# Performance work log

Hardware: AMD Instinct MI355X
Metric: run time of the kernel (lower is better)

Reference implementation:

```python
import jax, jax.numpy as jnp
import numpy as np

B, T, U, OUT_STEPS = 64, 128, 1024, 16


def setup_inputs() -> dict:
    key = jax.random.key(0)
    ks = jax.random.split(key, 8)
    s = 0.05  # small init scale to keep gates out of saturation
    return {
        "inputs": jax.random.normal(ks[0], (B, T, 1), jnp.float32),
        "k1": jax.random.normal(ks[1], (1, 4 * U), jnp.float32) * s,
        "r1": jax.random.normal(ks[2], (U, 4 * U), jnp.float32) * s,
        "b1": jnp.zeros((4 * U,), jnp.float32),
        "k2": jax.random.normal(ks[3], (U, 4 * U), jnp.float32) * s,
        "r2": jax.random.normal(ks[4], (U, 4 * U), jnp.float32) * s,
        "b2": jnp.zeros((4 * U,), jnp.float32),
        "wd": jax.random.normal(ks[5], (U, 1), jnp.float32) * s,
        "bd": jnp.zeros((1,), jnp.float32),
        "out_steps": OUT_STEPS,
    }


def _lstm(x_seq, h0, c0, Wx, Wh, b):
    """Keras-ordered (i,f,g,o) LSTM over a [B,T,D] sequence via lax.scan."""
    def step(carry, xt):
        h, c = carry
        z = xt @ Wx + h @ Wh + b  # [B, 4U]
        i, f, g, o = jnp.split(z, 4, axis=-1)
        c = jax.nn.sigmoid(f) * c + jax.nn.sigmoid(i) * jnp.tanh(g)
        h = jax.nn.sigmoid(o) * jnp.tanh(c)
        return (h, c), h
    (h, c), ys = jax.lax.scan(step, (h0, c0), jnp.swapaxes(x_seq, 0, 1))
    return jnp.swapaxes(ys, 0, 1), h, c  # seq [B,T,U], final h, c


def reference(inputs, k1, r1, b1, k2, r2, b2, wd, bd, out_steps):
    Bn = inputs.shape[0]
    Un = r1.shape[0]
    z0 = jnp.zeros((Bn, Un), inputs.dtype)
    # warmup: only lstm2's final states survive (faithful to the source code)
    x, _, _ = _lstm(inputs, z0, z0, k1, r1, b1)
    x, h, c = _lstm(x, z0, z0, k2, r2, b2)
    pred = x @ wd + bd  # [B, T, 1] (Dense applied to full sequence)
    preds = [pred]
    for _ in range(1, out_steps):
        # source quirk: lstm1 is seeded with lstm2's previous states,
        # lstm2 is seeded with lstm1's current states
        x, h1, c1 = _lstm(pred, h, c, k1, r1, b1)
        x, h, c = _lstm(x, h1, c1, k2, r2, b2)
        pred = x @ wd + bd
        preds.append(pred)
    return jnp.concatenate(preds, axis=1)  # [B, out_steps*T, 1]
```

## Files before the change

kernel.cpp:

```cpp
#include <hip/hip_runtime.h>
#include <cstdint>
#include <cstddef>

#define UU 1024
#define FOURU 4096
#define BATCH 64
#define TTT 128
#define SSS 16

typedef __attribute__((ext_vector_type(8))) short short8;
typedef __attribute__((ext_vector_type(4))) float f32x4;

__device__ __forceinline__ unsigned short f2bf(float f) {
    union { float f; uint32_t u; } v; v.f = f;
    uint32_t u = v.u;
    uint32_t r = (u + 0x7fffu + ((u >> 16) & 1u)) >> 16;
    return (unsigned short)r;
}
__device__ __forceinline__ float bf2f(unsigned short h) {
    union { uint32_t u; float f; } v; v.u = ((uint32_t)h) << 16;
    return v.f;
}

__global__ void repack_w1(const float* __restrict__ r1,
                          unsigned short* __restrict__ whi,
                          unsigned short* __restrict__ wlo) {
    int idx = blockIdx.x * 256 + threadIdx.x;
    int pc = idx >> 10, k = idx & 1023;
    int b = pc >> 4, g = (pc >> 2) & 3, j = pc & 3;
    int oc = g * UU + b * 4 + j;
    float v = r1[(size_t)k * FOURU + oc];
    unsigned short hi = f2bf(v);
    whi[idx] = hi;
    wlo[idx] = f2bf(v - bf2f(hi));
}

__global__ void repack_w2(const float* __restrict__ k2, const float* __restrict__ r2,
                          unsigned short* __restrict__ whi,
                          unsigned short* __restrict__ wlo) {
    int idx = blockIdx.x * 256 + threadIdx.x;
    int pc = idx >> 11, k = idx & 2047;
    int b = pc >> 4, g = (pc >> 2) & 3, j = pc & 3;
    int oc = g * UU + b * 4 + j;
    float v = (k < UU) ? k2[(size_t)k * FOURU + oc]
                       : r2[(size_t)(k - UU) * FOURU + oc];
    unsigned short hi = f2bf(v);
    whi[idx] = hi;
    wlo[idx] = f2bf(v - bf2f(hi));
}

template <int KTOT, bool IS1>
__global__ __launch_bounds__(256, 1) void cell_step(
    const unsigned short* __restrict__ Whi, const unsigned short* __restrict__ Wlo,
    const unsigned short* __restrict__ A1hi, const unsigned short* __restrict__ A1lo,
    const unsigned short* __restrict__ A2hi, const unsigned short* __restrict__ A2lo,
    const float* __restrict__ cin, float* __restrict__ cout,
    unsigned short* __restrict__ Hhi, unsigned short* __restrict__ Hlo,
    const float* __restrict__ bias,
    const float* __restrict__ k1, const float* __restrict__ xsrc, int xstride,
    int flags) {
    __shared__ float zp[4][64][16];
    const int tid = threadIdx.x;
    const int lane = tid & 63;
    const int w = tid >> 6;
    const int blk = blockIdx.x;
    constexpr int KSL = KTOT / 4;

    f32x4 acc[4] = {};

    bool skip;
    if (IS1) skip = (flags & 1) != 0;
    else     skip = ((flags & 1) != 0) && (w >= 2);

    if (!skip) {
        const int kbase = w * KSL;
        const unsigned short* Ah;
        const unsigned short* Al;
        int koff;
        if (KTOT == 2048 && kbase >= UU) { Ah = A2hi; Al = A2lo; koff = kbase - UU; }
        else                             { Ah = A1hi; Al = A1lo; koff = kbase; }
        const int kg8 = (lane >> 4) * 8;
        const int colpc = blk * 16 + (lane & 15);
        const unsigned short* wrh = Whi + (size_t)colpc * KTOT + kbase + kg8;
        const unsigned short* wrl = Wlo + (size_t)colpc * KTOT + kbase + kg8;

        for (int kk = 0; kk < KSL; kk += 32) {
            short8 bh = *(const short8*)(wrh + kk);
            short8 bl = *(const short8*)(wrl + kk);
#pragma unroll
            for (int m = 0; m < 4; ++m) {
                const int row = m * 16 + (lane & 15);
                const size_t aoff = (size_t)row * UU + koff + kk + kg8;
                short8 ah = *(const short8*)(Ah + aoff);
                short8 al = *(const short8*)(Al + aoff);
                acc[m] = __builtin_amdgcn_mfma_f32_16x16x32_bf16(ah, bh, acc[m], 0, 0, 0);
                acc[m] = __builtin_amdgcn_mfma_f32_16x16x32_bf16(al, bh, acc[m], 0, 0, 0);
                acc[m] = __builtin_amdgcn_mfma_f32_16x16x32_bf16(ah, bl, acc[m], 0, 0, 0);
            }
        }
    }

#pragma unroll
    for (int m = 0; m < 4; ++m) {
        const int rbase = m * 16 + (lane >> 4) * 4;
#pragma unroll
        for (int r = 0; r < 4; ++r)
            zp[w][rbase + r][lane & 15] = acc[m][r];
    }
    __syncthreads();

    {
        const int row = tid & 63;
        const int j = tid >> 6;
        float z[4];
#pragma unroll
        for (int g = 0; g < 4; ++g) {
            float s = 0.f;
#pragma unroll
            for (int ww = 0; ww < 4; ++ww) s += zp[ww][row][g * 4 + j];
            const int oc = g * UU + blk * 4 + j;
            s += bias[oc];
            if (IS1) {
                float xv = xsrc[(size_t)row * xstride];
                s += xv * k1[oc];
            }
            z[g] = s;
        }
        const int u = blk * 4 + j;
        float cold = (flags & 2) ? 0.f : cin[(size_t)row * UU + u];
        float ig = 1.f / (1.f + expf(-z[0]));
        float fg = 1.f / (1.f + expf(-z[1]));
        float gg = tanhf(z[2]);
        float og = 1.f / (1.f + expf(-z[3]));
        float cn = fg * cold + ig * gg;
        float hn = og * tanhf(cn);
        cout[(size_t)row * UU + u] = cn;
        unsigned short hh = f2bf(hn);
        Hhi[(size_t)row * UU + u] = hh;
        Hlo[(size_t)row * UU + u] = f2bf(hn - bf2f(hh));
    }
}

__global__ void dense_pred(const unsigned short* __restrict__ X2hi,
                           const unsigned short* __restrict__ X2lo,
                           const float* __restrict__ wd, const float* __restrict__ bd,
                           float* __restrict__ out) {
    const int gw = (blockIdx.x * 256 + threadIdx.x) >> 6;
    const int lane = threadIdx.x & 63;
    for (int d = gw; d < TTT * BATCH; d += 2048) {
        const int t = d >> 6, b = d & 63;
        const unsigned short* ph = X2hi + ((size_t)t * BATCH + b) * UU;
        const unsigned short* pl = X2lo + ((size_t)t * BATCH + b) * UU;
        float s = 0.f;
#pragma unroll 4
        for (int i = lane; i < UU; i += 64)
            s += (bf2f(ph[i]) + bf2f(pl[i])) * wd[i];
#pragma unroll
        for (int off = 32; off; off >>= 1) s += __shfl_down(s, off, 64);
        if (lane == 0) out[(size_t)b * (SSS * TTT) + t] = s + bd[0];
    }
}

extern "C" void kernel_launch(void* const* d_in, const int* in_sizes, int n_in,
                              void* d_out, int out_size, void* d_ws, size_t ws_size,
                              hipStream_t stream) {
    const float* inputs = (const float*)d_in[0];
    const float* k1     = (const float*)d_in[1];
    const float* r1     = (const float*)d_in[2];
    const float* b1     = (const float*)d_in[3];
    const float* k2     = (const float*)d_in[4];
    const float* r2     = (const float*)d_in[5];
    const float* b2     = (const float*)d_in[6];
    const float* wd     = (const float*)d_in[7];
    const float* bd     = (const float*)d_in[8];
    float* out = (float*)d_out;

    char* ws = (char*)d_ws;
    size_t off = 0;
    auto carve = [&](size_t bytes) -> void* {
        void* p = ws + off;
        off += (bytes + 255) & ~(size_t)255;
        return p;
    };
    const size_t BU = (size_t)BATCH * UU;
    unsigned short* W1hi = (unsigned short*)carve((size_t)FOURU * UU * 2);
    unsigned short* W1lo = (unsigned short*)carve((size_t)FOURU * UU * 2);
    unsigned short* W2hi = (unsigned short*)carve((size_t)FOURU * 2048 * 2);
    unsigned short* W2lo = (unsigned short*)carve((size_t)FOURU * 2048 * 2);
    unsigned short* X1hi = (unsigned short*)carve((size_t)TTT * BU * 2);
    unsigned short* X1lo = (unsigned short*)carve((size_t)TTT * BU * 2);
    unsigned short* X2hi = (unsigned short*)carve((size_t)TTT * BU * 2);
    unsigned short* X2lo = (unsigned short*)carve((size_t)TTT * BU * 2);
    float* c1 = (float*)carve(BU * 4);
    float* c2 = (float*)carve(BU * 4);

    repack_w1<<<dim3((FOURU * UU) / 256), dim3(256), 0, stream>>>(r1, W1hi, W1lo);
    repack_w2<<<dim3((FOURU * 2048) / 256), dim3(256), 0, stream>>>(k2, r2, W2hi, W2lo);

    for (int s = 0; s < SSS; ++s) {
        for (int t = 0; t < TTT; ++t) {
            const unsigned short *Ahi, *Alo;
            if (t == 0) { Ahi = X2hi + 127 * BU; Alo = X2lo + 127 * BU; }
            else        { Ahi = X1hi + (size_t)(t - 1) * BU; Alo = X1lo + (size_t)(t - 1) * BU; }
            const float* cinp = (t == 0) ? c2 : c1;
            int flags = (s == 0 && t == 0) ? 3 : 0;
            const float* xsrc;
            int xstride;
            if (s == 0) { xsrc = inputs + t; xstride = TTT; }
            else        { xsrc = out + (size_t)(s - 1) * TTT + t; xstride = SSS * TTT; }
            cell_step<1024, true><<<dim3(256), dim3(256), 0, stream>>>(
                W1hi, W1lo, Ahi, Alo, (const unsigned short*)nullptr, (const unsigned short*)nullptr,
                cinp, c1, X1hi + (size_t)t * BU, X1lo + (size_t)t * BU,
                b1, k1, xsrc, xstride, flags);
        }
        for (int t = 0; t < TTT; ++t) {
            const unsigned short *A2hi_, *A2lo_;
            if (t == 0) { A2hi_ = X1hi + 127 * BU; A2lo_ = X1lo + 127 * BU; }
            else        { A2hi_ = X2hi + (size_t)(t - 1) * BU; A2lo_ = X2lo + (size_t)(t - 1) * BU; }
            const float* cinp = (t == 0) ? c1 : c2;
            int flags = (s == 0 && t == 0) ? 3 : 0;
            cell_step<2048, false><<<dim3(256), dim3(256), 0, stream>>>(
                W2hi, W2lo,
                X1hi + (size_t)t * BU, X1lo + (size_t)t * BU, A2hi_, A2lo_,
                cinp, c2, X2hi + (size_t)t * BU, X2lo + (size_t)t * BU,
                b2, (const float*)nullptr, (const float*)nullptr, 0, flags);
        }
        dense_pred<<<dim3(512), dim3(256), 0, stream>>>(X2hi, X2lo, wd, bd,
                                                        out + (size_t)s * TTT);
    }
}
```

Before: 79.94 ms.

## Replace per-timestep launches with one persistent kernel using grid barriers

Replaces the ~4100 per-timestep kernel launches with a single persistent kernel of 256 blocks that loops over all steps, synchronising through an atomic grid barrier. The split-bf16 weight slices are kept in registers for the whole run instead of being reloaded from memory each step, and cell states move from global memory into registers. The dense prediction is folded into the same kernel. In exchange it needs all 256 blocks co-resident and holds 96 short8 vectors of weights per thread, which risks register spills, and the spin-based barrier adds latency on every step.

```diff
diff --git a/kernel.cpp b/kernel.cpp
--- a/kernel.cpp
+++ b/kernel.cpp
@@ -7,6 +7,8 @@
 #define BATCH 64
 #define TTT 128
 #define SSS 16
+#define BU 65536
+#define NBLK 256
 
 typedef __attribute__((ext_vector_type(8))) short short8;
 typedef __attribute__((ext_vector_type(4))) float f32x4;
@@ -20,6 +22,27 @@
 __device__ __forceinline__ float bf2f(unsigned short h) {
     union { uint32_t u; float f; } v; v.u = ((uint32_t)h) << 16;
     return v.f;
+}
+
+__device__ __forceinline__ void grid_barrier(unsigned int* bar) {
+    __syncthreads();
+    if (threadIdx.x == 0) {
+        unsigned int g = __hip_atomic_load(bar + 16, __ATOMIC_RELAXED, __HIP_MEMORY_SCOPE_AGENT);
+        unsigned int a = __hip_atomic_fetch_add(bar, 1u, __ATOMIC_ACQ_REL, __HIP_MEMORY_SCOPE_AGENT);
+        if (a == NBLK - 1u) {
+            __hip_atomic_store(bar, 0u, __ATOMIC_RELAXED, __HIP_MEMORY_SCOPE_AGENT);
+            __hip_atomic_store(bar + 16, g + 1u, __ATOMIC_RELEASE, __HIP_MEMORY_SCOPE_AGENT);
+        } else {
+            while (__hip_atomic_load(bar + 16, __ATOMIC_ACQUIRE, __HIP_MEMORY_SCOPE_AGENT) == g) {
+                __builtin_amdgcn_s_sleep(1);
+            }
+        }
+    }
+    __syncthreads();
+}
+
+__global__ void bar_init(unsigned int* bar) {
+    bar[threadIdx.x] = 0u;
 }
 
 __global__ void repack_w1(const float* __restrict__ r1,
@@ -49,115 +72,188 @@
     wlo[idx] = f2bf(v - bf2f(hi));
 }
 
-template <int KTOT, bool IS1>
-__global__ __launch_bounds__(256, 1) void cell_step(
-    const unsigned short* __restrict__ Whi, const unsigned short* __restrict__ Wlo,
-    const unsigned short* __restrict__ A1hi, const unsigned short* __restrict__ A1lo,
-    const unsigned short* __restrict__ A2hi, const unsigned short* __restrict__ A2lo,
-    const float* __restrict__ cin, float* __restrict__ cout,
-    unsigned short* __restrict__ Hhi, unsigned short* __restrict__ Hlo,
-    const float* __restrict__ bias,
-    const float* __restrict__ k1, const float* __restrict__ xsrc, int xstride,
-    int flags) {
+__global__ __launch_bounds__(256, 1) void feedback_persistent(
+    const unsigned short* __restrict__ W1hi, const unsigned short* __restrict__ W1lo,
+    const unsigned short* __restrict__ W2hi, const unsigned short* __restrict__ W2lo,
+    unsigned short* __restrict__ X1hi, unsigned short* __restrict__ X1lo,
+    unsigned short* __restrict__ X2hi, unsigned short* __restrict__ X2lo,
+    const float* __restrict__ inputs, const float* __restrict__ k1,
+    const float* __restrict__ b1, const float* __restrict__ b2,
+    const float* __restrict__ wd, const float* __restrict__ bd,
+    float* __restrict__ out, unsigned int* bar) {
     __shared__ float zp[4][64][16];
+
     const int tid = threadIdx.x;
     const int lane = tid & 63;
     const int w = tid >> 6;
     const int blk = blockIdx.x;
-    constexpr int KSL = KTOT / 4;
-
-    f32x4 acc[4] = {};
-
-    bool skip;
-    if (IS1) skip = (flags & 1) != 0;
-    else     skip = ((flags & 1) != 0) && (w >= 2);
-
-    if (!skip) {
-        const int kbase = w * KSL;
-        const unsigned short* Ah;
-        const unsigned short* Al;
-        int koff;
-        if (KTOT == 2048 && kbase >= UU) { Ah = A2hi; Al = A2lo; koff = kbase - UU; }
-        else                             { Ah = A1hi; Al = A1lo; koff = kbase; }
-        const int kg8 = (lane >> 4) * 8;
-        const int colpc = blk * 16 + (lane & 15);
-        const unsigned short* wrh = Whi + (size_t)colpc * KTOT + kbase + kg8;
-        const unsigned short* wrl = Wlo + (size_t)colpc * KTOT + kbase + kg8;
-
-        for (int kk = 0; kk < KSL; kk += 32) {
-            short8 bh = *(const short8*)(wrh + kk);
-            short8 bl = *(const short8*)(wrl + kk);
+    const int kg8 = (lane >> 4) * 8;
+    const int colpc = blk * 16 + (lane & 15);
+
+    short8 w1h[8], w1l[8], w2h[16], w2l[16];
+    {
+        const size_t base1 = (size_t)colpc * 1024 + (size_t)w * 256 + kg8;
+#pragma unroll
+        for (int i = 0; i < 8; ++i) {
+            w1h[i] = *(const short8*)(W1hi + base1 + i * 32);
+            w1l[i] = *(const short8*)(W1lo + base1 + i * 32);
+        }
+        const size_t base2 = (size_t)colpc * 2048 + (size_t)w * 512 + kg8;
+#pragma unroll
+        for (int i = 0; i < 16; ++i) {
+            w2h[i] = *(const short8*)(W2hi + base2 + i * 32);
+            w2l[i] = *(const short8*)(W2lo + base2 + i * 32);
+        }
+    }
+
+    const int erow = tid >> 2;
+    const int ej = tid & 3;
+    const int eu = blk * 4 + ej;
+    float b1v[4], b2v[4], k1v[4];
+#pragma unroll
+    for (int g = 0; g < 4; ++g) {
+        const int oc = g * UU + blk * 4 + ej;
+        b1v[g] = b1[oc];
+        b2v[g] = b2[oc];
+        k1v[g] = k1[oc];
+    }
+    float c1 = 0.f, c2 = 0.f;
+
+    const int gw = blk * 4 + w;
+
+    for (int s = 0; s < SSS; ++s) {
+        for (int t = 0; t < TTT; ++t) {
+            f32x4 acc[4] = {};
+            if (!(s == 0 && t == 0)) {
+                const unsigned short *Ah, *Al;
+                if (t == 0) { Ah = X2hi + 127 * BU; Al = X2lo + 127 * BU; }
+                else        { Ah = X1hi + (size_t)(t - 1) * BU; Al = X1lo + (size_t)(t - 1) * BU; }
+                const int koff = w * 256;
+#pragma unroll
+                for (int i = 0; i < 8; ++i) {
+                    const int kk = i * 32;
+#pragma unroll
+                    for (int m = 0; m < 4; ++m) {
+                        const int row = m * 16 + (lane & 15);
+                        const size_t aoff = (size_t)row * UU + koff + kk + kg8;
+                        short8 ah = *(const short8*)(Ah + aoff);
+                        short8 al = *(const short8*)(Al + aoff);
+                        acc[m] = __builtin_amdgcn_mfma_f32_16x16x32_bf16(ah, w1h[i], acc[m], 0, 0, 0);
+                        acc[m] = __builtin_amdgcn_mfma_f32_16x16x32_bf16(al, w1h[i], acc[m], 0, 0, 0);
+                        acc[m] = __builtin_amdgcn_mfma_f32_16x16x32_bf16(ah, w1l[i], acc[m], 0, 0, 0);
+                    }
+                }
+            }
 #pragma unroll
             for (int m = 0; m < 4; ++m) {
-                const int row = m * 16 + (lane & 15);
-                const size_t aoff = (size_t)row * UU + koff + kk + kg8;
-                short8 ah = *(const short8*)(Ah + aoff);
-                short8 al = *(const short8*)(Al + aoff);
-                acc[m] = __builtin_amdgcn_mfma_f32_16x16x32_bf16(ah, bh, acc[m], 0, 0, 0);
-                acc[m] = __builtin_amdgcn_mfma_f32_16x16x32_bf16(al, bh, acc[m], 0, 0, 0);
-                acc[m] = __builtin_amdgcn_mfma_f32_16x16x32_bf16(ah, bl, acc[m], 0, 0, 0);
-            }
-        }
-    }
-
-#pragma unroll
-    for (int m = 0; m < 4; ++m) {
-        const int rbase = m * 16 + (lane >> 4) * 4;
-#pragma unroll
-        for (int r = 0; r < 4; ++r)
-            zp[w][rbase + r][lane & 15] = acc[m][r];
-    }
-    __syncthreads();
-
-    {
-        const int row = tid & 63;
-        const int j = tid >> 6;
-        float z[4];
-#pragma unroll
-        for (int g = 0; g < 4; ++g) {
-            float s = 0.f;
-#pragma unroll
-            for (int ww = 0; ww < 4; ++ww) s += zp[ww][row][g * 4 + j];
-            const int oc = g * UU + blk * 4 + j;
-            s += bias[oc];
-            if (IS1) {
-                float xv = xsrc[(size_t)row * xstride];
-                s += xv * k1[oc];
-            }
-            z[g] = s;
-        }
-        const int u = blk * 4 + j;
-        float cold = (flags & 2) ? 0.f : cin[(size_t)row * UU + u];
-        float ig = 1.f / (1.f + expf(-z[0]));
-        float fg = 1.f / (1.f + expf(-z[1]));
-        float gg = tanhf(z[2]);
-        float og = 1.f / (1.f + expf(-z[3]));
-        float cn = fg * cold + ig * gg;
-        float hn = og * tanhf(cn);
-        cout[(size_t)row * UU + u] = cn;
-        unsigned short hh = f2bf(hn);
-        Hhi[(size_t)row * UU + u] = hh;
-        Hlo[(size_t)row * UU + u] = f2bf(hn - bf2f(hh));
-    }
-}
-
-__global__ void dense_pred(const unsigned short* __restrict__ X2hi,
-                           const unsigned short* __restrict__ X2lo,
-                           const float* __restrict__ wd, const float* __restrict__ bd,
-                           float* __restrict__ out) {
-    const int gw = (blockIdx.x * 256 + threadIdx.x) >> 6;
-    const int lane = threadIdx.x & 63;
-    for (int d = gw; d < TTT * BATCH; d += 2048) {
-        const int t = d >> 6, b = d & 63;
-        const unsigned short* ph = X2hi + ((size_t)t * BATCH + b) * UU;
-        const unsigned short* pl = X2lo + ((size_t)t * BATCH + b) * UU;
-        float s = 0.f;
+                const int rbase = m * 16 + (lane >> 4) * 4;
+#pragma unroll
+                for (int r = 0; r < 4; ++r)
+                    zp[w][rbase + r][lane & 15] = acc[m][r];
+            }
+            __syncthreads();
+            {
+                float xv = (s == 0) ? inputs[(size_t)erow * TTT + t]
+                                    : out[(size_t)erow * (SSS * TTT) + (s - 1) * TTT + t];
+                float z[4];
+#pragma unroll
+                for (int g = 0; g < 4; ++g) {
+                    float sum = zp[0][erow][g * 4 + ej] + zp[1][erow][g * 4 + ej] +
+                                zp[2][erow][g * 4 + ej] + zp[3][erow][g * 4 + ej];
+                    z[g] = sum + b1v[g] + xv * k1v[g];
+                }
+                float cold = (t == 0) ? c2 : c1;
+                float ig = 1.f / (1.f + expf(-z[0]));
+                float fg = 1.f / (1.f + expf(-z[1]));
+                float gg = tanhf(z[2]);
+                float og = 1.f / (1.f + expf(-z[3]));
+                float cn = fg * cold + ig * gg;
+                float hn = og * tanhf(cn);
+                c1 = cn;
+                unsigned short hh = f2bf(hn);
+                const size_t hoff = (size_t)t * BU + (size_t)erow * UU + eu;
+                X1hi[hoff] = hh;
+                X1lo[hoff] = f2bf(hn - bf2f(hh));
+            }
+            grid_barrier(bar);
+        }
+        for (int t = 0; t < TTT; ++t) {
+            f32x4 acc[4] = {};
+            const bool skiph = (s == 0 && t == 0);
+            {
+                const unsigned short *Ah, *Al;
+                int koff;
+                if (w < 2) {
+                    Ah = X1hi + (size_t)t * BU;
+                    Al = X1lo + (size_t)t * BU;
+                    koff = w * 512;
+                } else {
+                    if (t == 0) { Ah = X1hi + 127 * BU; Al = X1lo + 127 * BU; }
+                    else        { Ah = X2hi + (size_t)(t - 1) * BU; Al = X2lo + (size_t)(t - 1) * BU; }
+                    koff = (w - 2) * 512;
+                }
+                if (!(skiph && w >= 2)) {
+#pragma unroll
+                    for (int i = 0; i < 16; ++i) {
+                        const int kk = i * 32;
+#pragma unroll
+                        for (int m = 0; m < 4; ++m) {
+                            const int row = m * 16 + (lane & 15);
+                            const size_t aoff = (size_t)row * UU + koff + kk + kg8;
+                            short8 ah = *(const short8*)(Ah + aoff);
+                            short8 al = *(const short8*)(Al + aoff);
+                            acc[m] = __builtin_amdgcn_mfma_f32_16x16x32_bf16(ah, w2h[i], acc[m], 0, 0, 0);
+                            acc[m] = __builtin_amdgcn_mfma_f32_16x16x32_bf16(al, w2h[i], acc[m], 0, 0, 0);
+                            acc[m] = __builtin_amdgcn_mfma_f32_16x16x32_bf16(ah, w2l[i], acc[m], 0, 0, 0);
+                        }
+                    }
+                }
+            }
+#pragma unroll
+            for (int m = 0; m < 4; ++m) {
+                const int rbase = m * 16 + (lane >> 4) * 4;
+#pragma unroll
+                for (int r = 0; r < 4; ++r)
+                    zp[w][rbase + r][lane & 15] = acc[m][r];
+            }
+            __syncthreads();
+            {
+                float z[4];
+#pragma unroll
+                for (int g = 0; g < 4; ++g) {
+                    float sum = zp[0][erow][g * 4 + ej] + zp[1][erow][g * 4 + ej] +
+                                zp[2][erow][g * 4 + ej] + zp[3][erow][g * 4 + ej];
+                    z[g] = sum + b2v[g];
+                }
+                float cold = (t == 0) ? ((s == 0) ? 0.f : c1) : c2;
+                float ig = 1.f / (1.f + expf(-z[0]));
+                float fg = 1.f / (1.f + expf(-z[1]));
+                float gg = tanhf(z[2]);
+                float og = 1.f / (1.f + expf(-z[3]));
+                float cn = fg * cold + ig * gg;
+                float hn = og * tanhf(cn);
+                c2 = cn;
+                unsigned short hh = f2bf(hn);
+                const size_t hoff = (size_t)t * BU + (size_t)erow * UU + eu;
+                X2hi[hoff] = hh;
+                X2lo[hoff] = f2bf(hn - bf2f(hh));
+            }
+            grid_barrier(bar);
+        }
+        for (int i = 0; i < 8; ++i) {
+            const int d = gw + 1024 * i;
+            const int t = d >> 6, b = d & 63;
+            const unsigned short* ph = X2hi + (size_t)t * BU + (size_t)b * UU;
+            const unsigned short* pl = X2lo + (size_t)t * BU + (size_t)b * UU;
+            float ssum = 0.f;
 #pragma unroll 4
-        for (int i = lane; i < UU; i += 64)
-            s += (bf2f(ph[i]) + bf2f(pl[i])) * wd[i];
-#pragma unroll
-        for (int off = 32; off; off >>= 1) s += __shfl_down(s, off, 64);
-        if (lane == 0) out[(size_t)b * (SSS * TTT) + t] = s + bd[0];
+            for (int ii = lane; ii < UU; ii += 64)
+                ssum += (bf2f(ph[ii]) + bf2f(pl[ii])) * wd[ii];
+#pragma unroll
+            for (int off = 32; off; off >>= 1) ssum += __shfl_down(ssum, off, 64);
+            if (lane == 0) out[(size_t)b * (SSS * TTT) + s * TTT + t] = ssum + bd[0];
+        }
+        grid_barrier(bar);
     }
 }
 
@@ -182,7 +278,6 @@
         off += (bytes + 255) & ~(size_t)255;
         return p;
     };
-    const size_t BU = (size_t)BATCH * UU;
     unsigned short* W1hi = (unsigned short*)carve((size_t)FOURU * UU * 2);
     unsigned short* W1lo = (unsigned short*)carve((size_t)FOURU * UU * 2);
     unsigned short* W2hi = (unsigned short*)carve((size_t)FOURU * 2048 * 2);
@@ -191,41 +286,13 @@
     unsigned short* X1lo = (unsigned short*)carve((size_t)TTT * BU * 2);
     unsigned short* X2hi = (unsigned short*)carve((size_t)TTT * BU * 2);
     unsigned short* X2lo = (unsigned short*)carve((size_t)TTT * BU * 2);
-    float* c1 = (float*)carve(BU * 4);
-    float* c2 = (float*)carve(BU * 4);
-
+    unsigned int* bar = (unsigned int*)carve(256);
+
+    bar_init<<<dim3(1), dim3(64), 0, stream>>>(bar);
     repack_w1<<<dim3((FOURU * UU) / 256), dim3(256), 0, stream>>>(r1, W1hi, W1lo);
     repack_w2<<<dim3((FOURU * 2048) / 256), dim3(256), 0, stream>>>(k2, r2, W2hi, W2lo);
 
-    for (int s = 0; s < SSS; ++s) {
-        for (int t = 0; t < TTT; ++t) {
-            const unsigned short *Ahi, *Alo;
-            if (t == 0) { Ahi = X2hi + 127 * BU; Alo = X2lo + 127 * BU; }
-            else        { Ahi = X1hi + (size_t)(t - 1) * BU; Alo = X1lo + (size_t)(t - 1) * BU; }
-            const float* cinp = (t == 0) ? c2 : c1;
-            int flags = (s == 0 && t == 0) ? 3 : 0;
-            const float* xsrc;
-            int xstride;
-            if (s == 0) { xsrc = inputs + t; xstride = TTT; }
-            else        { xsrc = out + (size_t)(s - 1) * TTT + t; xstride = SSS * TTT; }
-            cell_step<1024, true><<<dim3(256), dim3(256), 0, stream>>>(
-                W1hi, W1lo, Ahi, Alo, (const unsigned short*)nullptr, (const unsigned short*)nullptr,
-                cinp, c1, X1hi + (size_t)t * BU, X1lo + (size_t)t * BU,
-                b1, k1, xsrc, xstride, flags);
-        }
-        for (int t = 0; t < TTT; ++t) {
-            const unsigned short *A2hi_, *A2lo_;
-            if (t == 0) { A2hi_ = X1hi + 127 * BU; A2lo_ = X1lo + 127 * BU; }
-            else        { A2hi_ = X2hi + (size_t)(t - 1) * BU; A2lo_ = X2lo + (size_t)(t - 1) * BU; }
-            const float* cinp = (t == 0) ? c1 : c2;
-            int flags = (s == 0 && t == 0) ? 3 : 0;
-            cell_step<2048, false><<<dim3(256), dim3(256), 0, stream>>>(
-                W2hi, W2lo,
-                X1hi + (size_t)t * BU, X1lo + (size_t)t * BU, A2hi_, A2lo_,
-                cinp, c2, X2hi + (size_t)t * BU, X2lo + (size_t)t * BU,
-                b2, (const float*)nullptr, (const float*)nullptr, 0, flags);
-        }
-        dense_pred<<<dim3(512), dim3(256), 0, stream>>>(X2hi, X2lo, wd, bd,
-                                                        out + (size_t)s * TTT);
-    }
-}
+    feedback_persistent<<<dim3(NBLK), dim3(256), 0, stream>>>(
+        W1hi, W1lo, W2hi, W2lo, X1hi, X1lo, X2hi, X2lo,
+        inputs, k1, b1, b2, wd, bd, out, bar);
+}
```

Result: slower. 167.1 ms (+109.1%).
